# Kernel optimization log

Measured on AMD Instinct MI355X. Metric: run time of the kernel, lower is better.

The kernel has to match this reference:

```python
import math
import jax, jax.numpy as jnp
import numpy as np

V, D, L, H, B, T = 50257, 1024, 6, 16, 4, 1024
HD = D // H  # 64


def layer_norm(x, s, b, eps=1e-5):
    m = jnp.mean(x, axis=-1, keepdims=True)
    v = jnp.var(x, axis=-1, keepdims=True)
    return (x - m) * jax.lax.rsqrt(v + eps) * s + b


def setup_inputs() -> dict:
    key = jax.random.key(0)
    ks = jax.random.split(key, 8)
    sc = 0.02
    return {
        "input_ids": jax.random.randint(ks[0], (B, T), 0, V),
        "attention_mask": jnp.ones((B, T), jnp.float32),
        "pool_mask": jax.random.uniform(ks[1], (B, T), dtype=jnp.float32),
        "embed": jax.random.normal(ks[2], (V, D), jnp.float32) * sc,
        "ln1_s": jnp.ones((L, D), jnp.float32),
        "ln1_b": jnp.zeros((L, D), jnp.float32),
        "qkv_w": jax.random.normal(ks[3], (L, D, 3 * D), jnp.float32) * sc,
        "qkv_b": jnp.zeros((L, 3 * D), jnp.float32),
        "attn_w": jax.random.normal(ks[4], (L, D, D), jnp.float32) * sc,
        "attn_b": jnp.zeros((L, D), jnp.float32),
        "ln2_s": jnp.ones((L, D), jnp.float32),
        "ln2_b": jnp.zeros((L, D), jnp.float32),
        "fc1_w": jax.random.normal(ks[5], (L, D, 4 * D), jnp.float32) * sc,
        "fc1_b": jnp.zeros((L, 4 * D), jnp.float32),
        "fc2_w": jax.random.normal(ks[6], (L, 4 * D, D), jnp.float32) * sc,
        "fc2_b": jnp.zeros((L, D), jnp.float32),
    }


def reference(input_ids, attention_mask, pool_mask, embed, ln1_s, ln1_b,
              qkv_w, qkv_b, attn_w, attn_b, ln2_s, ln2_b,
              fc1_w, fc1_b, fc2_w, fc2_b):
    h = embed[input_ids]  # [B,T,D]
    # key_mask.clamp(min=0) then log(clamp(min=1e-9)) == log(clip(mask, 1e-9))
    log_mask = jnp.log(jnp.clip(attention_mask, 1e-9))[:, None, None, :]  # [B,1,1,T]
    scale = 1.0 / math.sqrt(HD)

    def block(h, p):
        l1s, l1b, qw, qb, aw, ab, l2s, l2b, f1w, f1b, f2w, f2b = p
        x = layer_norm(h, l1s, l1b)
        qkv = jnp.einsum('btd,de->bte', x, qw) + qb          # [B,T,3D]
        qkv = qkv.reshape(B, T, H, 3 * HD).transpose(0, 2, 1, 3)  # [B,H,T,3hd]
        q, k, v = jnp.split(qkv, 3, axis=-1)
        scores = jnp.einsum('bhqd,bhkd->bhqk', q, k) * scale + log_mask
        probs = jax.nn.softmax(scores, axis=-1)
        ctx = jnp.einsum('bhqk,bhkd->bhqd', probs, v)
        ctx = ctx.transpose(0, 2, 1, 3).reshape(B, T, D)
        h = h + jnp.einsum('btd,de->bte', ctx, aw) + ab
        y = layer_norm(h, l2s, l2b)
        y = jax.nn.gelu(jnp.einsum('btd,df->btf', y, f1w) + f1b, approximate=False)
        h = h + jnp.einsum('btf,fd->btd', y, f2w) + f2b
        # NOTE: source applies post_attention_layernorm a second time at block end
        h = layer_norm(h, l2s, l2b)
        return h, None

    params = (ln1_s, ln1_b, qkv_w, qkv_b, attn_w, attn_b,
              ln2_s, ln2_b, fc1_w, fc1_b, fc2_w, fc2_b)
    h, _ = jax.lax.scan(block, h, params)

    # pool with pool_mask, then L2-normalize (F.normalize, eps=1e-12)
    m = pool_mask[..., None]
    sent = (h * m).sum(axis=1) / jnp.clip(m.sum(axis=1), 1e-6)
    return sent / jnp.clip(jnp.linalg.norm(sent, axis=-1, keepdims=True), 1e-12)
```

## Files before the change

### kernel.cpp

```cpp
#include <hip/hip_runtime.h>
#include <hip/hip_bf16.h>
#include <math.h>

#define VV 50257
#define DD 1024
#define LL 6
#define HH 16
#define BB 4
#define TT 1024
#define HD 64
#define BT (BB*TT)

typedef __attribute__((ext_vector_type(8))) short bf16x8;
typedef __attribute__((ext_vector_type(8))) _Float16 f16x8;
typedef __attribute__((ext_vector_type(4))) float f32x4;
typedef __attribute__((ext_vector_type(16))) float f32x16;

__device__ inline float b2f(unsigned short u) {
    unsigned x = ((unsigned)u) << 16;
    return __uint_as_float(x);
}
__device__ inline unsigned short f2b(float f) {
    __hip_bfloat16 h = __float2bfloat16(f);
    return *reinterpret_cast<unsigned short*>(&h);
}
__device__ inline void plswap32(unsigned &dst, unsigned &src) {
    asm("v_permlane32_swap_b32 %0, %1" : "+v"(dst), "+v"(src));
}

#define GLOAD16(g, l) __builtin_amdgcn_global_load_lds( \
    (const __attribute__((address_space(1))) void*)(g), \
    (__attribute__((address_space(3))) void*)(l), 16, 0, 0)

__device__ inline float block_sum_256(float v, float* ws) {
    #pragma unroll
    for (int o = 32; o > 0; o >>= 1) v += __shfl_down(v, o);
    const int lane = threadIdx.x & 63, wid = threadIdx.x >> 6;
    if (lane == 0) ws[wid] = v;
    __syncthreads();
    return ws[0] + ws[1] + ws[2] + ws[3];
}

__launch_bounds__(256)
__global__ void gather_ln(const int* __restrict__ ids, const float* __restrict__ emb,
                          float* __restrict__ h, unsigned short* __restrict__ xb,
                          const float* __restrict__ g, const float* __restrict__ bta) {
    __shared__ float ws1[4], ws2[4];
    const int row = blockIdx.x, tid = threadIdx.x;
    const int id = ids[row];
    const int d = tid * 4;
    float4 v = *(const float4*)(emb + (size_t)id * DD + d);
    *(float4*)(h + (size_t)row * DD + d) = v;
    float s = v.x + v.y + v.z + v.w;
    float m = block_sum_256(s, ws1) * (1.0f / 1024.0f);
    float d0 = v.x - m, d1 = v.y - m, d2 = v.z - m, d3 = v.w - m;
    float s2 = d0*d0 + d1*d1 + d2*d2 + d3*d3;
    float rstd = rsqrtf(block_sum_256(s2, ws2) * (1.0f / 1024.0f) + 1e-5f);
    float4 gg = *(const float4*)(g + d);
    float4 bb = *(const float4*)(bta + d);
    ushort4 o;
    o.x = f2b(d0 * rstd * gg.x + bb.x);
    o.y = f2b(d1 * rstd * gg.y + bb.y);
    o.z = f2b(d2 * rstd * gg.z + bb.z);
    o.w = f2b(d3 * rstd * gg.w + bb.w);
    *(ushort4*)(xb + (size_t)row * DD + d) = o;
}

__launch_bounds__(256)
__global__ void logmask_k(const float* __restrict__ am, float* __restrict__ lm) {
    int i = blockIdx.x * 256 + threadIdx.x;
    if (i < BT) lm[i] = logf(fmaxf(am[i], 1e-9f));
}

__launch_bounds__(256)
__global__ void ln_f32(const float* __restrict__ in, float* __restrict__ out,
                       const float* __restrict__ g, const float* __restrict__ bta) {
    __shared__ float ws1[4], ws2[4];
    const int row = blockIdx.x, tid = threadIdx.x;
    const float* x = in + (size_t)row * DD;
    float4 v = *(const float4*)(x + tid * 4);
    float s = v.x + v.y + v.z + v.w;
    float m = block_sum_256(s, ws1) * (1.0f / 1024.0f);
    float d0 = v.x - m, d1 = v.y - m, d2 = v.z - m, d3 = v.w - m;
    float s2 = d0*d0 + d1*d1 + d2*d2 + d3*d3;
    float rstd = rsqrtf(block_sum_256(s2, ws2) * (1.0f / 1024.0f) + 1e-5f);
    const int d = tid * 4;
    float4 gg = *(const float4*)(g + d);
    float4 bb = *(const float4*)(bta + d);
    float4 o;
    o.x = d0 * rstd * gg.x + bb.x;
    o.y = d1 * rstd * gg.y + bb.y;
    o.z = d2 * rstd * gg.z + bb.z;
    o.w = d3 * rstd * gg.w + bb.w;
    *(float4*)(out + (size_t)row * DD + d) = o;
}

__launch_bounds__(256)
__global__ void ln_bf16(const float* __restrict__ in, unsigned short* __restrict__ out,
                        const float* __restrict__ g, const float* __restrict__ bta) {
    __shared__ float ws1[4], ws2[4];
    const int row = blockIdx.x, tid = threadIdx.x;
    const float* x = in + (size_t)row * DD;
    float4 v = *(const float4*)(x + tid * 4);
    float s = v.x + v.y + v.z + v.w;
    float m = block_sum_256(s, ws1) * (1.0f / 1024.0f);
    float d0 = v.x - m, d1 = v.y - m, d2 = v.z - m, d3 = v.w - m;
    float s2 = d0*d0 + d1*d1 + d2*d2 + d3*d3;
    float rstd = rsqrtf(block_sum_256(s2, ws2) * (1.0f / 1024.0f) + 1e-5f);
    const int d = tid * 4;
    float4 gg = *(const float4*)(g + d);
    float4 bb = *(const float4*)(bta + d);
    ushort4 o;
    o.x = f2b(d0 * rstd * gg.x + bb.x);
    o.y = f2b(d1 * rstd * gg.y + bb.y);
    o.z = f2b(d2 * rstd * gg.z + bb.z);
    o.w = f2b(d3 * rstd * gg.w + bb.w);
    *(ushort4*)(out + (size_t)row * DD + d) = o;
}

__launch_bounds__(256)
__global__ void ln_dual(const float* __restrict__ in, float* __restrict__ outf,
                        const float* __restrict__ g2, const float* __restrict__ b2v,
                        unsigned short* __restrict__ outb,
                        const float* __restrict__ g1, const float* __restrict__ b1v) {
    __shared__ float ws1[4], ws2[4], ws3[4], ws4[4];
    const int row = blockIdx.x, tid = threadIdx.x;
    const int d = tid * 4;
    float4 v = *(const float4*)(in + (size_t)row * DD + d);
    float s = v.x + v.y + v.z + v.w;
    float m = block_sum_256(s, ws1) * (1.0f / 1024.0f);
    float d0 = v.x - m, d1 = v.y - m, d2 = v.z - m, d3 = v.w - m;
    float s2 = d0*d0 + d1*d1 + d2*d2 + d3*d3;
    float rstd = rsqrtf(block_sum_256(s2, ws2) * (1.0f / 1024.0f) + 1e-5f);
    float4 gg = *(const float4*)(g2 + d);
    float4 bb = *(const float4*)(b2v + d);
    float4 y;
    y.x = d0 * rstd * gg.x + bb.x;
    y.y = d1 * rstd * gg.y + bb.y;
    y.z = d2 * rstd * gg.z + bb.z;
    y.w = d3 * rstd * gg.w + bb.w;
    *(float4*)(outf + (size_t)row * DD + d) = y;
    float t = y.x + y.y + y.z + y.w;
    float m2 = block_sum_256(t, ws3) * (1.0f / 1024.0f);
    float e0 = y.x - m2, e1 = y.y - m2, e2 = y.z - m2, e3 = y.w - m2;
    float t2 = e0*e0 + e1*e1 + e2*e2 + e3*e3;
    float rstd2 = rsqrtf(block_sum_256(t2, ws4) * (1.0f / 1024.0f) + 1e-5f);
    float4 g1v = *(const float4*)(g1 + d);
    float4 b1x = *(const float4*)(b1v + d);
    ushort4 o;
    o.x = f2b(e0 * rstd2 * g1v.x + b1x.x);
    o.y = f2b(e1 * rstd2 * g1v.y + b1x.y);
    o.z = f2b(e2 * rstd2 * g1v.z + b1x.z);
    o.w = f2b(e3 * rstd2 * g1v.w + b1x.w);
    *(ushort4*)(outb + (size_t)row * DD + d) = o;
}

__launch_bounds__(256)
__global__ void wtrans_all(const float* __restrict__ wq, unsigned short* __restrict__ wqo,
                           const float* __restrict__ wa, unsigned short* __restrict__ wao,
                           const float* __restrict__ w1, unsigned short* __restrict__ w1o,
                           const float* __restrict__ w2, unsigned short* __restrict__ w2o) {
    __shared__ float tile[64][65];
    const int l = blockIdx.x / 3072;
    int id = blockIdx.x % 3072;
    const float* W; unsigned short* Wt; int K, N, tx, ty;
    if (id < 768)       { W = wq + (size_t)l*1024*3072; Wt = wqo + (size_t)l*3072*1024; K = 1024; N = 3072; tx = id % 48; ty = id / 48; }
    else if (id < 1024) { id -= 768;  W = wa + (size_t)l*1024*1024; Wt = wao + (size_t)l*1024*1024; K = 1024; N = 1024; tx = id & 15; ty = id >> 4; }
    else if (id < 2048) { id -= 1024; W = w1 + (size_t)l*1024*4096; Wt = w1o + (size_t)l*4096*1024; K = 1024; N = 4096; tx = id & 63; ty = id >> 6; }
    else                { id -= 2048; W = w2 + (size_t)l*4096*1024; Wt = w2o + (size_t)l*1024*4096; K = 4096; N = 1024; tx = id & 15; ty = id >> 4; }
    const int k0 = ty * 64, n0 = tx * 64;
    const int lrow = threadIdx.x >> 4;
    const int lcol = (threadIdx.x & 15) * 4;
    #pragma unroll
    for (int i = 0; i < 4; ++i) {
        const int r = lrow + i * 16;
        *(float4*)&tile[r][lcol] = *(const float4*)(W + (size_t)(k0 + r) * N + n0 + lcol);
    }
    __syncthreads();
    #pragma unroll
    for (int i = 0; i < 4; ++i) {
        const int n = lrow + i * 16;
        ushort4 o;
        o.x = f2b(tile[lcol + 0][n]);
        o.y = f2b(tile[lcol + 1][n]);
        o.z = f2b(tile[lcol + 2][n]);
        o.w = f2b(tile[lcol + 3][n]);
        *(ushort4*)(Wt + (size_t)(n0 + n) * K + k0 + lcol) = o;
    }
}

#define BM 128
#define BK 32

__device__ inline float gelu_f(float v) {
    return 0.5f * v * (1.0f + erff(v * 0.70710678118654752f));
}

template<int EPI, int NFRAG>
__launch_bounds__(256)
__global__ void gemm_mfma(const unsigned short* __restrict__ A,
                          const unsigned short* __restrict__ Bt,
                          const float* __restrict__ bias, void* __restrict__ Cv,
                          int M, int K, int N) {
    constexpr int BN = NFRAG * 32;
    constexpr int BG = NFRAG / 2;
    __shared__ short As[2][BM * BK];
    __shared__ short Bs[2][BN * BK];

    const int tid = threadIdx.x;
    const int wid = tid >> 6, lane = tid & 63;

    const int nwg = gridDim.x * gridDim.y;
    int bid = blockIdx.y * gridDim.x + blockIdx.x;
    bid = (bid & 7) * (nwg >> 3) + (bid >> 3);
    const int m0 = (bid / gridDim.x) * BM;
    const int n0 = (bid % gridDim.x) * BN;

    const int wr = wid >> 1, wc = wid & 1;
    const int fr = lane & 15, fq = lane >> 4;

    const int rowS = tid >> 2;
    const int blkS = tid & 3;
    const int swz0 = (rowS >> 1) & 3;
    const unsigned short* aS0 = A  + (size_t)(m0 + rowS)      * K + (blkS ^ swz0) * 8;
    const unsigned short* aS1 = A  + (size_t)(m0 + rowS + 64) * K + (blkS ^ swz0) * 8;
    const unsigned short* bS0 = Bt + (size_t)(n0 + rowS)      * K + (blkS ^ swz0) * 8;
    const unsigned short* bS1 = Bt + (size_t)(n0 + rowS + 64) * K + (blkS ^ swz0) * 8;

    const int sF = (fr >> 1) & 3;
    int aoff[4], boff[NFRAG];
    #pragma unroll
    for (int m = 0; m < 4; ++m) aoff[m] = (wr * 64 + m * 16 + fr) * BK + ((fq ^ sF) * 8);
    #pragma unroll
    for (int n = 0; n < NFRAG; ++n) boff[n] = (wc * (NFRAG * 16) + n * 16 + fr) * BK + ((fq ^ sF) * 8);

    f32x4 acc[4][NFRAG];
    #pragma unroll
    for (int m = 0; m < 4; ++m)
        #pragma unroll
        for (int n = 0; n < NFRAG; ++n) acc[m][n] = (f32x4){0.f, 0.f, 0.f, 0.f};

    const int T = K / BK;

    GLOAD16(aS0, &As[0][(wid * 64) * 8]);
    GLOAD16(aS1, &As[0][(256 + wid * 64) * 8]);
    GLOAD16(bS0, &Bs[0][(wid * 64) * 8]);
    if (BG > 1) GLOAD16(bS1, &Bs[0][(256 + wid * 64) * 8]);

    int cur = 0;
    for (int t = 0; t < T; ++t) {
        __syncthreads();
        if (t + 1 < T) {
            const int nb = cur ^ 1;
            const size_t ko = (size_t)(t + 1) * BK;
            GLOAD16(aS0 + ko, &As[nb][(wid * 64) * 8]);
            GLOAD16(aS1 + ko, &As[nb][(256 + wid * 64) * 8]);
            GLOAD16(bS0 + ko, &Bs[nb][(wid * 64) * 8]);
            if (BG > 1) GLOAD16(bS1 + ko, &Bs[nb][(256 + wid * 64) * 8]);
        }
        bf16x8 af[4], bfr[NFRAG];
        #pragma unroll
        for (int m = 0; m < 4; ++m) af[m] = *(const bf16x8*)&As[cur][aoff[m]];
        #pragma unroll
        for (int n = 0; n < NFRAG; ++n) bfr[n] = *(const bf16x8*)&Bs[cur][boff[n]];
        #pragma unroll
        for (int m = 0; m < 4; ++m)
            #pragma unroll
            for (int n = 0; n < NFRAG; ++n)
                acc[m][n] = __builtin_amdgcn_mfma_f32_16x16x32_bf16(
                    af[m], bfr[n], acc[m][n], 0, 0, 0);
        cur ^= 1;
    }

    float bias_v[NFRAG];
    #pragma unroll
    for (int n = 0; n < NFRAG; ++n) bias_v[n] = bias[n0 + wc * (NFRAG * 16) + n * 16 + fr];

    #pragma unroll
    for (int m = 0; m < 4; ++m) {
        #pragma unroll
        for (int n = 0; n < NFRAG; ++n) {
            const int col = n0 + wc * (NFRAG * 16) + n * 16 + fr;
            #pragma unroll
            for (int j = 0; j < 4; ++j) {
                const int row = m0 + wr * 64 + m * 16 + fq * 4 + j;
                float v = acc[m][n][j] + bias_v[n];
                if (EPI == 1) {
                    float* C = (float*)Cv;
                    C[(size_t)row * N + col] += v;
                } else {
                    if (EPI == 2) v = gelu_f(v);
                    unsigned short* C = (unsigned short*)Cv;
                    C[(size_t)row * N + col] = f2b(v);
                }
            }
        }
    }
}

__launch_bounds__(256)
__global__ void attn_mfma(const unsigned short* __restrict__ qkv,
                          const float* __restrict__ lm,
                          unsigned short* __restrict__ ctx) {
    int bid = blockIdx.x;
    const int ww = (bid & 7) * 64 + (bid >> 3);
    const int bh = ww >> 3, qt = ww & 7;
    const int b = bh >> 4, hh = bh & 15;
    const int tid = threadIdx.x, w = tid >> 6, lane = tid & 63;
    const int lo = lane & 31, hf = lane >> 5;
    const int q_row = qt * 128 + w * 32 + lo;

    __shared__ short Ks[2][64 * 64];
    __shared__ short Vt[2][64 * 72];
    __shared__ float lms[2][64];

    bf16x8 qf[4];
    {
        const unsigned short* qbase = qkv + (size_t)(b * TT + q_row) * 3072 + hh * 192;
        #pragma unroll
        for (int kk = 0; kk < 4; ++kk)
            qf[kk] = *(const bf16x8*)(qbase + (2 * kk + hf) * 8);
    }

    const int r0 = tid >> 3, cS = tid & 7;
    const unsigned short* kp = qkv + (size_t)(b * TT + r0) * 3072 + hh * 192 + 64
                               + ((cS ^ (r0 & 7)) * 8);
    const int vkey = tid & 31, vc = tid >> 5;
    const unsigned short* vp = qkv + (size_t)(b * TT + vkey) * 3072 + hh * 192 + 128 + vc * 8;
    const float* lmrow = lm + b * TT;

    f32x16 o0, o1;
    #pragma unroll
    for (int j = 0; j < 16; ++j) { o0[j] = 0.f; o1[j] = 0.f; }
    float M = -1e30f, S = 0.f;

    {
        GLOAD16(kp, &Ks[0][(w * 64) * 8]);
        GLOAD16(kp + (size_t)32 * 3072, &Ks[0][(256 + w * 64) * 8]);
        bf16x8 v0 = *(const bf16x8*)vp;
        bf16x8 v1 = *(const bf16x8*)(vp + (size_t)32 * 3072);
        if (tid < 64) lms[0][tid] = lmrow[tid];
        #pragma unroll
        for (int i = 0; i < 8; ++i) {
            _Float16 h0 = (_Float16)b2f((unsigned short)v0[i]);
            _Float16 h1 = (_Float16)b2f((unsigned short)v1[i]);
            Vt[0][(vc * 8 + i) * 72 + vkey] = *reinterpret_cast<short*>(&h0);
            Vt[0][(vc * 8 + i) * 72 + 32 + vkey] = *reinterpret_cast<short*>(&h1);
        }
    }

    int cur = 0;
    for (int kt = 0; kt < 16; ++kt) {
        __syncthreads();
        if (kt < 15) {
            const int nb = cur ^ 1;
            const size_t off = (size_t)((kt + 1) * 64) * 3072;
            GLOAD16(kp + off, &Ks[nb][(w * 64) * 8]);
            GLOAD16(kp + off + (size_t)32 * 3072, &Ks[nb][(256 + w * 64) * 8]);
            bf16x8 v0 = *(const bf16x8*)(vp + off);
            bf16x8 v1 = *(const bf16x8*)(vp + off + (size_t)32 * 3072);
            if (tid < 64) lms[nb][tid] = lmrow[(kt + 1) * 64 + tid];
            #pragma unroll
            for (int i = 0; i < 8; ++i) {
                _Float16 h0 = (_Float16)b2f((unsigned short)v0[i]);
                _Float16 h1 = (_Float16)b2f((unsigned short)v1[i]);
                Vt[nb][(vc * 8 + i) * 72 + vkey] = *reinterpret_cast<short*>(&h0);
                Vt[nb][(vc * 8 + i) * 72 + 32 + vkey] = *reinterpret_cast<short*>(&h1);
            }
        }

        #pragma unroll
        for (int g = 0; g < 2; ++g) {
            f32x16 s16;
            #pragma unroll
            for (int j = 0; j < 16; ++j) s16[j] = 0.f;
            __builtin_amdgcn_s_setprio(1);
            #pragma unroll
            for (int kk = 0; kk < 4; ++kk) {
                const int c = (2 * kk + hf) ^ (lo & 7);
                bf16x8 kf = *(const bf16x8*)&Ks[cur][((g * 32 + lo) * 8 + c) * 8];
                s16 = __builtin_amdgcn_mfma_f32_32x32x16_bf16(kf, qf[kk], s16, 0, 0, 0);
            }
            __builtin_amdgcn_s_setprio(0);

            float p[16];
            float mx = -1e30f;
            #pragma unroll
            for (int j = 0; j < 16; ++j) {
                const int kidx = g * 32 + (j & 3) + 8 * (j >> 2) + 4 * hf;
                float sv = s16[j] * 0.125f + lms[cur][kidx];
                p[j] = sv;
                mx = fmaxf(mx, sv);
            }
            mx = fmaxf(mx, __shfl_xor(mx, 32));
            if (!__all(mx <= M + 8.0f)) {
                const float Mn = fmaxf(M, mx);
                const float f = __expf(M - Mn);
                S *= f;
                #pragma unroll
                for (int j = 0; j < 16; ++j) { o0[j] *= f; o1[j] *= f; }
                M = Mn;
            }

            unsigned short ph[16];
            float ls = 0.f;
            #pragma unroll
            for (int j = 0; j < 16; ++j) {
                _Float16 hq = (_Float16)__expf(p[j] - M);
                ph[j] = *reinterpret_cast<unsigned short*>(&hq);
                ls += (float)hq;
            }
            ls += __shfl_xor(ls, 32);
            S += ls;

            unsigned ra = (unsigned)ph[0]  | ((unsigned)ph[1]  << 16);
            unsigned rb = (unsigned)ph[2]  | ((unsigned)ph[3]  << 16);
            unsigned rc = (unsigned)ph[4]  | ((unsigned)ph[5]  << 16);
            unsigned rd = (unsigned)ph[6]  | ((unsigned)ph[7]  << 16);
            unsigned re = (unsigned)ph[8]  | ((unsigned)ph[9]  << 16);
            unsigned rf = (unsigned)ph[10] | ((unsigned)ph[11] << 16);
            unsigned rg = (unsigned)ph[12] | ((unsigned)ph[13] << 16);
            unsigned rh = (unsigned)ph[14] | ((unsigned)ph[15] << 16);
            plswap32(ra, rc);
            plswap32(rb, rd);
            plswap32(re, rg);
            plswap32(rf, rh);
            union { unsigned u[4]; f16x8 v; } p1, p2;
            p1.u[0] = ra; p1.u[1] = rb; p1.u[2] = rc; p1.u[3] = rd;
            p2.u[0] = re; p2.u[1] = rf; p2.u[2] = rg; p2.u[3] = rh;

            f16x8 va0 = *(const f16x8*)&Vt[cur][lo * 72 + g * 32 + hf * 8];
            f16x8 va1 = *(const f16x8*)&Vt[cur][lo * 72 + g * 32 + 16 + hf * 8];
            f16x8 vb0 = *(const f16x8*)&Vt[cur][(32 + lo) * 72 + g * 32 + hf * 8];
            f16x8 vb1 = *(const f16x8*)&Vt[cur][(32 + lo) * 72 + g * 32 + 16 + hf * 8];
            __builtin_amdgcn_s_setprio(1);
            o0 = __builtin_amdgcn_mfma_f32_32x32x16_f16(va0, p1.v, o0, 0, 0, 0);
            o0 = __builtin_amdgcn_mfma_f32_32x32x16_f16(va1, p2.v, o0, 0, 0, 0);
            o1 = __builtin_amdgcn_mfma_f32_32x32x16_f16(vb0, p1.v, o1, 0, 0, 0);
            o1 = __builtin_amdgcn_mfma_f32_32x32x16_f16(vb1, p2.v, o1, 0, 0, 0);
            __builtin_amdgcn_s_setprio(0);
        }
        cur ^= 1;
    }

    const float inv = 1.f / S;
    unsigned short* obase = ctx + (size_t)(b * TT + q_row) * DD + hh * 64;
    #pragma unroll
    for (int g = 0; g < 4; ++g) {
        const int dbase = 8 * g + 4 * hf;
        ushort4 w0, w1;
        w0.x = f2b(o0[4*g+0] * inv); w0.y = f2b(o0[4*g+1] * inv);
        w0.z = f2b(o0[4*g+2] * inv); w0.w = f2b(o0[4*g+3] * inv);
        w1.x = f2b(o1[4*g+0] * inv); w1.y = f2b(o1[4*g+1] * inv);
        w1.z = f2b(o1[4*g+2] * inv); w1.w = f2b(o1[4*g+3] * inv);
        *(ushort4*)(obase + dbase) = w0;
        *(ushort4*)(obase + 32 + dbase) = w1;
    }
}

__launch_bounds__(256)
__global__ void pool_partial(const float* __restrict__ h, const float* __restrict__ pm,
                             float* __restrict__ part) {
    const int b = blockIdx.x >> 4, c = blockIdx.x & 15;
    const int tid = threadIdx.x;
    const float* hp = h + (size_t)(b * TT + c * 64) * DD + tid * 4;
    const float* pp = pm + b * TT + c * 64;
    float4 acc = {0.f, 0.f, 0.f, 0.f};
    for (int t = 0; t < 64; ++t) {
        const float p = pp[t];
        float4 v = *(const float4*)(hp + (size_t)t * DD);
        acc.x += p * v.x; acc.y += p * v.y; acc.z += p * v.z; acc.w += p * v.w;
    }
    *(float4*)(part + (size_t)blockIdx.x * DD + tid * 4) = acc;
}

__launch_bounds__(1024)
__global__ void pool_final(const float* __restrict__ part, const float* __restrict__ pm,
                           float* __restrict__ out) {
    const int b = blockIdx.x, d = threadIdx.x;
    __shared__ float ws[16];
    float s = pm[b * TT + d];
    #pragma unroll
    for (int o = 32; o > 0; o >>= 1) s += __shfl_down(s, o);
    if ((d & 63) == 0) ws[d >> 6] = s;
    __syncthreads();
    float msum = 0.f;
    #pragma unroll
    for (int i = 0; i < 16; ++i) msum += ws[i];

    float acc = 0.f;
    #pragma unroll
    for (int c = 0; c < 16; ++c)
        acc += part[(size_t)(b * 16 + c) * DD + d];
    const float sent = acc / fmaxf(msum, 1e-6f);

    float qv = sent * sent;
    #pragma unroll
    for (int o = 32; o > 0; o >>= 1) qv += __shfl_down(qv, o);
    __syncthreads();
    if ((d & 63) == 0) ws[d >> 6] = qv;
    __syncthreads();
    float nrm = 0.f;
    #pragma unroll
    for (int i = 0; i < 16; ++i) nrm += ws[i];
    nrm = sqrtf(nrm);
    out[b * DD + d] = sent / fmaxf(nrm, 1e-12f);
}

extern "C" void kernel_launch(void* const* d_in, const int* in_sizes, int n_in,
                              void* d_out, int out_size, void* d_ws, size_t ws_size,
                              hipStream_t stream) {
    const int*   ids    = (const int*)  d_in[0];
    const float* amask  = (const float*)d_in[1];
    const float* pmask  = (const float*)d_in[2];
    const float* embed  = (const float*)d_in[3];
    const float* ln1_s  = (const float*)d_in[4];
    const float* ln1_b  = (const float*)d_in[5];
    const float* qkv_w  = (const float*)d_in[6];
    const float* qkv_b  = (const float*)d_in[7];
    const float* attn_w = (const float*)d_in[8];
    const float* attn_b = (const float*)d_in[9];
    const float* ln2_s  = (const float*)d_in[10];
    const float* ln2_b  = (const float*)d_in[11];
    const float* fc1_w  = (const float*)d_in[12];
    const float* fc1_b  = (const float*)d_in[13];
    const float* fc2_w  = (const float*)d_in[14];
    const float* fc2_b  = (const float*)d_in[15];

    char* wp = (char*)d_ws;
    float* h = (float*)wp;                 wp += (size_t)BT * DD * 4;
    unsigned short* qkv_bf = (unsigned short*)wp; wp += (size_t)BT * 3072 * 2;
    unsigned short* act_bf = (unsigned short*)wp; wp += (size_t)BT * 4096 * 2;
    unsigned short* x_bf   = (unsigned short*)wp; wp += (size_t)BT * DD * 2;
    unsigned short* wq_t   = (unsigned short*)wp; wp += (size_t)LL * 3072 * 1024 * 2;
    unsigned short* wa_t   = (unsigned short*)wp; wp += (size_t)LL * 1024 * 1024 * 2;
    unsigned short* w1_t   = (unsigned short*)wp; wp += (size_t)LL * 4096 * 1024 * 2;
    unsigned short* w2_t   = (unsigned short*)wp; wp += (size_t)LL * 1024 * 4096 * 2;
    float* lm = (float*)wp;                wp += (size_t)BT * 4;
    float* part = (float*)wp;              wp += (size_t)64 * DD * 4;

    gather_ln<<<BT, 256, 0, stream>>>(ids, embed, h, x_bf, ln1_s, ln1_b);
    logmask_k<<<16, 256, 0, stream>>>(amask, lm);
    wtrans_all<<<LL * 3072, 256, 0, stream>>>(qkv_w, wq_t, attn_w, wa_t,
                                              fc1_w, w1_t, fc2_w, w2_t);

    for (int l = 0; l < LL; ++l) {
        const size_t lD = (size_t)l * DD;
        const unsigned short* wq = wq_t + (size_t)l * 3072 * 1024;
        const unsigned short* wa = wa_t + (size_t)l * 1024 * 1024;
        const unsigned short* w1 = w1_t + (size_t)l * 4096 * 1024;
        const unsigned short* w2 = w2_t + (size_t)l * 1024 * 4096;

        gemm_mfma<0, 4><<<dim3(3072/128, BT/BM), 256, 0, stream>>>(
            x_bf, wq, qkv_b + (size_t)l * 3072, qkv_bf, BT, 1024, 3072);
        attn_mfma<<<512, 256, 0, stream>>>(qkv_bf, lm, x_bf);
        gemm_mfma<1, 2><<<dim3(1024/64, BT/BM), 256, 0, stream>>>(
            x_bf, wa, attn_b + lD, h, BT, 1024, 1024);
        ln_bf16<<<BT, 256, 0, stream>>>(h, x_bf, ln2_s + lD, ln2_b + lD);
        gemm_mfma<2, 4><<<dim3(4096/128, BT/BM), 256, 0, stream>>>(
            x_bf, w1, fc1_b + (size_t)l * 4096, act_bf, BT, 1024, 4096);
        gemm_mfma<1, 2><<<dim3(1024/64, BT/BM), 256, 0, stream>>>(
            act_bf, w2, fc2_b + lD, h, BT, 4096, 1024);

        if (l < LL - 1) {
            ln_dual<<<BT, 256, 0, stream>>>(h, h, ln2_s + lD, ln2_b + lD,
                                            x_bf, ln1_s + lD + DD, ln1_b + lD + DD);
        } else {
            ln_f32<<<BT, 256, 0, stream>>>(h, h, ln2_s + lD, ln2_b + lD);
        }
    }

    pool_partial<<<64, 256, 0, stream>>>(h, pmask, part);
    pool_final<<<BB, 1024, 0, stream>>>(part, pmask, (float*)d_out);
}
```

Measured before the change: 1.751 ms.

## Widen GEMM K-tile to 64 with single-buffered LDS, batch weight transpose

The GEMM K-step grows from 32 to 64 with a new 8-chunk XOR swizzle, which halves the number of loop iterations and barriers. In exchange, the double-buffered LDS prefetch is replaced by a single buffer with a load-then-sync pattern, so global loads no longer overlap MFMA work. The weight transpose kernel now handles four 64-row K tiles per block, prefetching the next tile into registers. The log-mask computation is folded into the embedding gather/LN kernel to save one launch.

After: 1.763 ms. Within noise of the previous version (+0.7%).

```diff
diff --git a/kernel.cpp b/kernel.cpp
--- a/kernel.cpp
+++ b/kernel.cpp
@@ -44,11 +44,13 @@
 __launch_bounds__(256)
 __global__ void gather_ln(const int* __restrict__ ids, const float* __restrict__ emb,
                           float* __restrict__ h, unsigned short* __restrict__ xb,
-                          const float* __restrict__ g, const float* __restrict__ bta) {
+                          const float* __restrict__ g, const float* __restrict__ bta,
+                          const float* __restrict__ am, float* __restrict__ lm) {
     __shared__ float ws1[4], ws2[4];
     const int row = blockIdx.x, tid = threadIdx.x;
     const int id = ids[row];
     const int d = tid * 4;
+    if (tid == 0) lm[row] = logf(fmaxf(am[row], 1e-9f));
     float4 v = *(const float4*)(emb + (size_t)id * DD + d);
     *(float4*)(h + (size_t)row * DD + d) = v;
     float s = v.x + v.y + v.z + v.w;
@@ -64,12 +66,6 @@
     o.z = f2b(d2 * rstd * gg.z + bb.z);
     o.w = f2b(d3 * rstd * gg.w + bb.w);
     *(ushort4*)(xb + (size_t)row * DD + d) = o;
-}
-
-__launch_bounds__(256)
-__global__ void logmask_k(const float* __restrict__ am, float* __restrict__ lm) {
-    int i = blockIdx.x * 256 + threadIdx.x;
-    if (i < BT) lm[i] = logf(fmaxf(am[i], 1e-9f));
 }
 
 __launch_bounds__(256)
@@ -161,36 +157,51 @@
                            const float* __restrict__ w1, unsigned short* __restrict__ w1o,
                            const float* __restrict__ w2, unsigned short* __restrict__ w2o) {
     __shared__ float tile[64][65];
-    const int l = blockIdx.x / 3072;
-    int id = blockIdx.x % 3072;
-    const float* W; unsigned short* Wt; int K, N, tx, ty;
-    if (id < 768)       { W = wq + (size_t)l*1024*3072; Wt = wqo + (size_t)l*3072*1024; K = 1024; N = 3072; tx = id % 48; ty = id / 48; }
-    else if (id < 1024) { id -= 768;  W = wa + (size_t)l*1024*1024; Wt = wao + (size_t)l*1024*1024; K = 1024; N = 1024; tx = id & 15; ty = id >> 4; }
-    else if (id < 2048) { id -= 1024; W = w1 + (size_t)l*1024*4096; Wt = w1o + (size_t)l*4096*1024; K = 1024; N = 4096; tx = id & 63; ty = id >> 6; }
-    else                { id -= 2048; W = w2 + (size_t)l*4096*1024; Wt = w2o + (size_t)l*1024*4096; K = 4096; N = 1024; tx = id & 15; ty = id >> 4; }
-    const int k0 = ty * 64, n0 = tx * 64;
+    const int l = blockIdx.x / 768;
+    int id = blockIdx.x % 768;
+    const float* W; unsigned short* Wt; int K, N, tn, tk;
+    if (id < 192)      { W = wq + (size_t)l*1024*3072; Wt = wqo + (size_t)l*3072*1024; K = 1024; N = 3072; tn = id % 48; tk = id / 48; }
+    else if (id < 256) { id -= 192; W = wa + (size_t)l*1024*1024; Wt = wao + (size_t)l*1024*1024; K = 1024; N = 1024; tn = id & 15; tk = id >> 4; }
+    else if (id < 512) { id -= 256; W = w1 + (size_t)l*1024*4096; Wt = w1o + (size_t)l*4096*1024; K = 1024; N = 4096; tn = id & 63; tk = id >> 6; }
+    else               { id -= 512; W = w2 + (size_t)l*4096*1024; Wt = w2o + (size_t)l*1024*4096; K = 4096; N = 1024; tn = id & 15; tk = id >> 4; }
+    const int n0 = tn * 64;
+    const int k0 = tk * 256;
     const int lrow = threadIdx.x >> 4;
     const int lcol = (threadIdx.x & 15) * 4;
-    #pragma unroll
-    for (int i = 0; i < 4; ++i) {
-        const int r = lrow + i * 16;
-        *(float4*)&tile[r][lcol] = *(const float4*)(W + (size_t)(k0 + r) * N + n0 + lcol);
-    }
-    __syncthreads();
-    #pragma unroll
-    for (int i = 0; i < 4; ++i) {
-        const int n = lrow + i * 16;
-        ushort4 o;
-        o.x = f2b(tile[lcol + 0][n]);
-        o.y = f2b(tile[lcol + 1][n]);
-        o.z = f2b(tile[lcol + 2][n]);
-        o.w = f2b(tile[lcol + 3][n]);
-        *(ushort4*)(Wt + (size_t)(n0 + n) * K + k0 + lcol) = o;
+
+    float4 r[4];
+    #pragma unroll
+    for (int i = 0; i < 4; ++i)
+        r[i] = *(const float4*)(W + (size_t)(k0 + lrow + i * 16) * N + n0 + lcol);
+
+    for (int s = 0; s < 4; ++s) {
+        __syncthreads();
+        #pragma unroll
+        for (int i = 0; i < 4; ++i)
+            *(float4*)&tile[lrow + i * 16][lcol] = r[i];
+        if (s < 3) {
+            const int k1 = k0 + (s + 1) * 64;
+            #pragma unroll
+            for (int i = 0; i < 4; ++i)
+                r[i] = *(const float4*)(W + (size_t)(k1 + lrow + i * 16) * N + n0 + lcol);
+        }
+        __syncthreads();
+        const int kb = k0 + s * 64;
+        #pragma unroll
+        for (int i = 0; i < 4; ++i) {
+            const int n = lrow + i * 16;
+            ushort4 o;
+            o.x = f2b(tile[lcol + 0][n]);
+            o.y = f2b(tile[lcol + 1][n]);
+            o.z = f2b(tile[lcol + 2][n]);
+            o.w = f2b(tile[lcol + 3][n]);
+            *(ushort4*)(Wt + (size_t)(n0 + n) * K + kb + lcol) = o;
+        }
     }
 }
 
 #define BM 128
-#define BK 32
+#define BK 64
 
 __device__ inline float gelu_f(float v) {
     return 0.5f * v * (1.0f + erff(v * 0.70710678118654752f));
@@ -203,9 +214,8 @@
                           const float* __restrict__ bias, void* __restrict__ Cv,
                           int M, int K, int N) {
     constexpr int BN = NFRAG * 32;
-    constexpr int BG = NFRAG / 2;
-    __shared__ short As[2][BM * BK];
-    __shared__ short Bs[2][BN * BK];
+    __shared__ short As[BM * BK];
+    __shared__ short Bs[BN * BK];
 
     const int tid = threadIdx.x;
     const int wid = tid >> 6, lane = tid & 63;
@@ -219,20 +229,20 @@
     const int wr = wid >> 1, wc = wid & 1;
     const int fr = lane & 15, fq = lane >> 4;
 
-    const int rowS = tid >> 2;
-    const int blkS = tid & 3;
-    const int swz0 = (rowS >> 1) & 3;
-    const unsigned short* aS0 = A  + (size_t)(m0 + rowS)      * K + (blkS ^ swz0) * 8;
-    const unsigned short* aS1 = A  + (size_t)(m0 + rowS + 64) * K + (blkS ^ swz0) * 8;
-    const unsigned short* bS0 = Bt + (size_t)(n0 + rowS)      * K + (blkS ^ swz0) * 8;
-    const unsigned short* bS1 = Bt + (size_t)(n0 + rowS + 64) * K + (blkS ^ swz0) * 8;
-
-    const int sF = (fr >> 1) & 3;
+    const int rowS = tid >> 3;
+    const int cS = tid & 7;
+    const int coff = (cS ^ (rowS & 7)) * 8;
+    const unsigned short* aS = A  + (size_t)(m0 + rowS) * K + coff;
+    const unsigned short* bS = Bt + (size_t)(n0 + rowS) * K + coff;
+    const size_t rstride = (size_t)32 * K;
+
+    const int key = fr & 7;
+    const int c0 = fq ^ key;
     int aoff[4], boff[NFRAG];
     #pragma unroll
-    for (int m = 0; m < 4; ++m) aoff[m] = (wr * 64 + m * 16 + fr) * BK + ((fq ^ sF) * 8);
-    #pragma unroll
-    for (int n = 0; n < NFRAG; ++n) boff[n] = (wc * (NFRAG * 16) + n * 16 + fr) * BK + ((fq ^ sF) * 8);
+    for (int m = 0; m < 4; ++m) aoff[m] = (wr * 64 + m * 16 + fr) * BK + c0 * 8;
+    #pragma unroll
+    for (int n = 0; n < NFRAG; ++n) boff[n] = (wc * (NFRAG * 16) + n * 16 + fr) * BK + c0 * 8;
 
     f32x4 acc[4][NFRAG];
     #pragma unroll
@@ -240,36 +250,29 @@
         #pragma unroll
         for (int n = 0; n < NFRAG; ++n) acc[m][n] = (f32x4){0.f, 0.f, 0.f, 0.f};
 
-    const int T = K / BK;
-
-    GLOAD16(aS0, &As[0][(wid * 64) * 8]);
-    GLOAD16(aS1, &As[0][(256 + wid * 64) * 8]);
-    GLOAD16(bS0, &Bs[0][(wid * 64) * 8]);
-    if (BG > 1) GLOAD16(bS1, &Bs[0][(256 + wid * 64) * 8]);
-
-    int cur = 0;
-    for (int t = 0; t < T; ++t) {
+    for (int kk = 0; kk < K; kk += BK) {
         __syncthreads();
-        if (t + 1 < T) {
-            const int nb = cur ^ 1;
-            const size_t ko = (size_t)(t + 1) * BK;
-            GLOAD16(aS0 + ko, &As[nb][(wid * 64) * 8]);
-            GLOAD16(aS1 + ko, &As[nb][(256 + wid * 64) * 8]);
-            GLOAD16(bS0 + ko, &Bs[nb][(wid * 64) * 8]);
-            if (BG > 1) GLOAD16(bS1 + ko, &Bs[nb][(256 + wid * 64) * 8]);
-        }
-        bf16x8 af[4], bfr[NFRAG];
-        #pragma unroll
-        for (int m = 0; m < 4; ++m) af[m] = *(const bf16x8*)&As[cur][aoff[m]];
-        #pragma unroll
-        for (int n = 0; n < NFRAG; ++n) bfr[n] = *(const bf16x8*)&Bs[cur][boff[n]];
-        #pragma unroll
-        for (int m = 0; m < 4; ++m)
-            #pragma unroll
-            for (int n = 0; n < NFRAG; ++n)
-                acc[m][n] = __builtin_amdgcn_mfma_f32_16x16x32_bf16(
-                    af[m], bfr[n], acc[m][n], 0, 0, 0);
-        cur ^= 1;
+        #pragma unroll
+        for (int r = 0; r < 4; ++r)
+            GLOAD16(aS + kk + r * rstride, &As[(wid * 64 + r * 256) * 8]);
+        #pragma unroll
+        for (int r = 0; r < NFRAG; ++r)
+            GLOAD16(bS + kk + r * rstride, &Bs[(wid * 64 + r * 256) * 8]);
+        __syncthreads();
+        #pragma unroll
+        for (int s = 0; s < 2; ++s) {
+            bf16x8 af[4], bfr[NFRAG];
+            #pragma unroll
+            for (int m = 0; m < 4; ++m) af[m] = *(const bf16x8*)&As[aoff[m] ^ (s << 5)];
+            #pragma unroll
+            for (int n = 0; n < NFRAG; ++n) bfr[n] = *(const bf16x8*)&Bs[boff[n] ^ (s << 5)];
+            #pragma unroll
+            for (int m = 0; m < 4; ++m)
+                #pragma unroll
+                for (int n = 0; n < NFRAG; ++n)
+                    acc[m][n] = __builtin_amdgcn_mfma_f32_16x16x32_bf16(
+                        af[m], bfr[n], acc[m][n], 0, 0, 0);
+        }
     }
 
     float bias_v[NFRAG];
@@ -539,10 +542,9 @@
     float* lm = (float*)wp;                wp += (size_t)BT * 4;
     float* part = (float*)wp;              wp += (size_t)64 * DD * 4;
 
-    gather_ln<<<BT, 256, 0, stream>>>(ids, embed, h, x_bf, ln1_s, ln1_b);
-    logmask_k<<<16, 256, 0, stream>>>(amask, lm);
-    wtrans_all<<<LL * 3072, 256, 0, stream>>>(qkv_w, wq_t, attn_w, wa_t,
-                                              fc1_w, w1_t, fc2_w, w2_t);
+    gather_ln<<<BT, 256, 0, stream>>>(ids, embed, h, x_bf, ln1_s, ln1_b, amask, lm);
+    wtrans_all<<<LL * 768, 256, 0, stream>>>(qkv_w, wq_t, attn_w, wa_t,
+                                             fc1_w, w1_t, fc2_w, w2_t);
 
     for (int l = 0; l < LL; ++l) {
         const size_t lD = (size_t)l * DD;
```
